# Performance work log

Measured on AMD Instinct MI355X. Metric: run time of the kernel, lower is better.

Reference implementation:

```python
import jax, jax.numpy as jnp
import numpy as np

EPS = 1e-5

def _bn(h):
    # BatchNorm1d, affine=False, track_running_stats=False -> batch stats, biased var
    m = h.mean(axis=0)
    v = h.var(axis=0)
    return (h - m) * jax.lax.rsqrt(v + EPS)

def _aggregate(x, edge_index):
    # out[i] = sum over edges (i <- j) of x[j]  + x[i] (self loop)
    dst, src = edge_index[0], edge_index[1]
    n = x.shape[0]
    return jax.ops.segment_sum(x[src], dst, num_segments=n) + x

def setup_inputs() -> dict:
    key = jax.random.key(0)
    ks = jax.random.split(key, 12)
    N, F, H, C, E = 100000, 128, 128, 40, 800000
    x = jax.random.normal(ks[0], (N, F), dtype=jnp.float32)
    edge_index = jax.random.randint(ks[1], (2, E), 0, N, dtype=jnp.int64)
    def lin(kw, kb, fan_in, fan_out):
        bound = 1.0 / np.sqrt(fan_in)
        W = jax.random.uniform(kw, (fan_in, fan_out), minval=-bound, maxval=bound, dtype=jnp.float32)
        b = jax.random.uniform(kb, (fan_out,), minval=-bound, maxval=bound, dtype=jnp.float32)
        return W, b
    W0, b0 = lin(ks[2], ks[3], F, H)
    W1, b1 = lin(ks[4], ks[5], H, H)
    W2, b2 = lin(ks[6], ks[7], H, H)
    Wl, bl = lin(ks[8], ks[9], H, C)
    return {"x": x, "edge_index": edge_index, "W0": W0, "b0": b0,
            "W1": W1, "b1": b1, "W2": W2, "b2": b2, "Wl": Wl, "bl": bl}

def reference(x, edge_index, W0, b0, W1, b1, W2, b2, Wl, bl):
    h = x
    for W, b in ((W0, b0), (W1, b1), (W2, b2)):
        h = _aggregate(h, edge_index)          # spmm(A + I, h)
        h = h @ W + b                          # Linear
        h = _bn(h)                             # BatchNorm1d (no affine)
        h = jax.nn.relu(h)
    return h @ Wl + bl
```

## Files before the change

kernel.cpp:

```cpp
#include <hip/hip_runtime.h>
#include <stdint.h>

typedef __attribute__((ext_vector_type(8))) short short8;
typedef __attribute__((ext_vector_type(4))) float floatx4;

static __device__ __forceinline__ float b2f(uint16_t b){
    return __uint_as_float(((uint32_t)b) << 16);
}
static __device__ __forceinline__ uint16_t f2b(float f){
    uint32_t u = __float_as_uint(f);
    return (uint16_t)((u + 0x7fffu + ((u >> 16) & 1u)) >> 16);
}
static __device__ __forceinline__ float blo(uint32_t v){ return __uint_as_float(v << 16); }
static __device__ __forceinline__ float bhi(uint32_t v){ return __uint_as_float(v & 0xffff0000u); }
static __device__ __forceinline__ uint32_t pack2(float a, float b){
    return ((uint32_t)f2b(b) << 16) | (uint32_t)f2b(a);
}

__global__ void k_sentinel(uint32_t* out, int nwords, uint32_t pat){
    int i = blockIdx.x * blockDim.x + threadIdx.x;
    if (i < nwords) out[i] = pat;
}

__global__ void k_zf(int* deg, int N, const uint32_t* xw, const int* ei, int* flags,
                     float* stats, int ZB){
    if ((int)blockIdx.x == ZB){
        if (threadIdx.x != 0) return;
        int odd_nz = 0;
        for (int k = 0; k < 128; k++){
            if (ei[2 * k + 1] != 0) odd_nz = 1;
        }
        flags[0] = odd_nz ? 0 : 1;
        int big = 0;
        for (int k = 0; k < 128; k++){
            float lo = __uint_as_float(xw[k] << 16);
            if (!(fabsf(lo) <= 1024.0f)) big = 1;
        }
        flags[1] = big ? 0 : 1;
        return;
    }
    if ((int)blockIdx.x == ZB + 1){
        int t = threadIdx.x;
        #pragma unroll
        for (int j = 0; j < 3; j++) stats[j * 256 + t] = 0.f;
        return;
    }
    int i = blockIdx.x * blockDim.x + threadIdx.x;
    if (i < N) deg[i] = 0;
}

__global__ void k_deg(const int* ei, int E, int* deg, uint16_t* rank, const int* flags){
    int e = blockIdx.x * blockDim.x + threadIdx.x;
    if (e < E){
        int d = flags[0] ? ei[2 * e] : ei[e];
        int r = atomicAdd(&deg[d], 1);
        rank[e] = (uint16_t)r;
    }
}

__global__ void k_scan1(const int* deg, int N, int* bsum){
    __shared__ int s[256];
    int t = threadIdx.x;
    int i = blockIdx.x * 256 + t;
    s[t] = (i < N) ? deg[i] : 0;
    __syncthreads();
    for (int off = 128; off > 0; off >>= 1){
        if (t < off) s[t] += s[t + off];
        __syncthreads();
    }
    if (t == 0) bsum[blockIdx.x] = s[0];
}

__global__ void k_scan2(int* bsum, int nb, int* rp, int N){
    __shared__ int s[512];
    int t = threadIdx.x;
    int v = (t < nb) ? bsum[t] : 0;
    s[t] = v;
    __syncthreads();
    for (int off = 1; off < 512; off <<= 1){
        int u = (t >= off) ? s[t - off] : 0;
        __syncthreads();
        s[t] += u;
        __syncthreads();
    }
    if (t < nb) bsum[t] = s[t] - v;
    if (t == 511) rp[N] = s[511];
}

__global__ void k_scan3(const int* deg, int N, const int* bpre, int* rp){
    __shared__ int s[256];
    int t = threadIdx.x;
    int i = blockIdx.x * 256 + t;
    int v = (i < N) ? deg[i] : 0;
    s[t] = v;
    __syncthreads();
    for (int off = 1; off < 256; off <<= 1){
        int u = (t >= off) ? s[t - off] : 0;
        __syncthreads();
        s[t] += u;
        __syncthreads();
    }
    if (i < N) rp[i] = bpre[blockIdx.x] + s[t] - v;
}

__global__ __launch_bounds__(256) void k_fill(const int* __restrict__ ei, int E,
                                              const int* __restrict__ rp,
                                              const uint16_t* __restrict__ rank,
                                              int* __restrict__ col,
                                              const int* __restrict__ flags, int N){
    int xcd = blockIdx.x & 7;
    int sub = blockIdx.x >> 3;
    int nsub = gridDim.x >> 3;
    int r0 = (int)(((long long)N * xcd) >> 3);
    int r1 = (int)(((long long)N * (xcd + 1)) >> 3);
    int e0 = (int)(((long long)E * sub) / nsub);
    int e1 = (int)(((long long)E * (sub + 1)) / nsub);
    int is64 = flags[0];
    for (int e = e0 + threadIdx.x; e < e1; e += 256){
        int d = is64 ? ei[2 * e] : ei[e];
        if (d >= r0 && d < r1){
            int sv = is64 ? ei[2 * (E + e)] : ei[E + e];
            int p = rp[d] + (int)rank[e];
            col[p] = sv;
        }
    }
}

__global__ void k_prep(const void* W0, const void* W1, const void* W2, const void* Wl,
                       uint16_t* Wf0, uint16_t* Wf1, uint16_t* Wf2, uint16_t* Wfl,
                       const void* b0, const void* b1, const void* b2, const void* bl,
                       float* bc, const void* x, uint16_t* hx, int N,
                       const int* flags){
    int blk = blockIdx.x;
    int t = threadIdx.x;
    if (blk >= 218){
        int nb = gridDim.x - 218;
        int bi = blk - 218;
        int half2 = N * 2;
        int isbf = flags[1];
        for (int c = 0; c < 8; c++){
            uint4* dst = (uint4*)(hx + (size_t)c * N * 16);
            if (isbf){
                const uint16_t* xb = (const uint16_t*)x;
                for (int idx = bi * 256 + t; idx < half2; idx += nb * 256){
                    int row = idx >> 1, h = idx & 1;
                    dst[idx] = *(const uint4*)(xb + (size_t)row * 128 + c * 16 + h * 8);
                }
            } else {
                const float* xf = (const float*)x;
                for (int idx = bi * 256 + t; idx < half2; idx += nb * 256){
                    int row = idx >> 1, h = idx & 1;
                    const float4* s = (const float4*)(xf + (size_t)row * 128 + c * 16 + h * 8);
                    float4 u0 = s[0];
                    float4 u1 = s[1];
                    uint4 o;
                    o.x = pack2(u0.x, u0.y); o.y = pack2(u0.z, u0.w);
                    o.z = pack2(u1.x, u1.y); o.w = pack2(u1.z, u1.w);
                    dst[idx] = o;
                }
            }
        }
        return;
    }
    if (blk >= 216){
        int i = (blk - 216) * 256 + t;
        if (i >= 424) return;
        const void* src; int li;
        if (i < 128)      { src = b0; li = i; }
        else if (i < 256) { src = b1; li = i - 128; }
        else if (i < 384) { src = b2; li = i - 256; }
        else              { src = bl; li = i - 384; }
        bc[i] = flags[1] ? b2f(((const uint16_t*)src)[li]) : ((const float*)src)[li];
        return;
    }
    const void* W; uint16_t* Wf; int C, ntiles, lb;
    if (blk < 64)        { W = W0; Wf = Wf0; C = 128; ntiles = 8; lb = blk; }
    else if (blk < 128)  { W = W1; Wf = Wf1; C = 128; ntiles = 8; lb = blk - 64; }
    else if (blk < 192)  { W = W2; Wf = Wf2; C = 128; ntiles = 8; lb = blk - 128; }
    else                 { W = Wl; Wf = Wfl; C = 40;  ntiles = 3; lb = blk - 192; }
    int idx = lb * 256 + t;
    int total = 4 * ntiles * 512;
    if (idx >= total) return;
    int j = idx & 7;
    int lane = (idx >> 3) & 63;
    int nt = (idx >> 9) % ntiles;
    int kt = idx / (512 * ntiles);
    int k = kt * 32 + (lane >> 4) * 8 + j;
    int n = nt * 16 + (lane & 15);
    uint16_t v = 0;
    if (n < C){
        v = flags[1] ? ((const uint16_t*)W)[k * C + n]
                     : f2b(((const float*)W)[k * C + n]);
    }
    Wf[idx] = v;
}

__global__ __launch_bounds__(256) void k_aggc(const uint16_t* __restrict__ Yin,
                                              const int* __restrict__ rp,
                                              const int* __restrict__ col,
                                              uint16_t* __restrict__ out,
                                              int N, int RT,
                                              const float* __restrict__ st,
                                              int apply_bn, float ninv){
    int t = threadIdx.x;
    int c = blockIdx.x & 7;
    int tile = blockIdx.x >> 3;
    int r = t >> 1, h = t & 1;
    int i = tile * 128 + r;
    if (i >= N) return;
    float tt[8], iv[8];
    if (apply_bn){
        int f0 = c * 16 + h * 8;
        #pragma unroll
        for (int j = 0; j < 8; j++){
            float sv = st[f0 + j];
            float qv = st[128 + f0 + j];
            float m = sv * ninv;
            float var = qv * ninv - m * m;
            float ivj = rsqrtf(var + 1e-5f);
            iv[j] = ivj;
            tt[j] = -m * ivj;
        }
    }
    const uint4* base = (const uint4*)(Yin + (size_t)c * N * 16);
    int s0 = rp[i], e0 = rp[i + 1];
    float a[8];
    {
        uint4 w = base[(size_t)i * 2 + h];
        a[0] = blo(w.x); a[1] = bhi(w.x); a[2] = blo(w.y); a[3] = bhi(w.y);
        a[4] = blo(w.z); a[5] = bhi(w.z); a[6] = blo(w.w); a[7] = bhi(w.w);
        if (apply_bn){
            #pragma unroll
            for (int jj = 0; jj < 8; jj++) a[jj] = fmaxf(fmaf(a[jj], iv[jj], tt[jj]), 0.f);
        }
    }
    int k = s0;
    for (; k + 3 < e0; k += 4){
        int j0 = col[k], j1 = col[k + 1], j2 = col[k + 2], j3 = col[k + 3];
        uint4 ww[4];
        ww[0] = base[(size_t)j0 * 2 + h];
        ww[1] = base[(size_t)j1 * 2 + h];
        ww[2] = base[(size_t)j2 * 2 + h];
        ww[3] = base[(size_t)j3 * 2 + h];
        #pragma unroll
        for (int u = 0; u < 4; u++){
            float v[8] = {blo(ww[u].x), bhi(ww[u].x), blo(ww[u].y), bhi(ww[u].y),
                          blo(ww[u].z), bhi(ww[u].z), blo(ww[u].w), bhi(ww[u].w)};
            if (apply_bn){
                #pragma unroll
                for (int jj = 0; jj < 8; jj++) v[jj] = fmaxf(fmaf(v[jj], iv[jj], tt[jj]), 0.f);
            }
            #pragma unroll
            for (int jj = 0; jj < 8; jj++) a[jj] += v[jj];
        }
    }
    for (; k < e0; k++){
        int j = col[k];
        uint4 w = base[(size_t)j * 2 + h];
        float v[8] = {blo(w.x), bhi(w.x), blo(w.y), bhi(w.y),
                      blo(w.z), bhi(w.z), blo(w.w), bhi(w.w)};
        if (apply_bn){
            #pragma unroll
            for (int jj = 0; jj < 8; jj++) v[jj] = fmaxf(fmaf(v[jj], iv[jj], tt[jj]), 0.f);
        }
        #pragma unroll
        for (int jj = 0; jj < 8; jj++) a[jj] += v[jj];
    }
    uint4 o;
    o.x = pack2(a[0], a[1]); o.y = pack2(a[2], a[3]);
    o.z = pack2(a[4], a[5]); o.w = pack2(a[6], a[7]);
    ((uint4*)(out + (size_t)c * N * 16))[(size_t)i * 2 + h] = o;
}

__global__ __launch_bounds__(256) void k_gemm(uint16_t* __restrict__ A,
                                              const uint16_t* __restrict__ Wf,
                                              const float* __restrict__ bias,
                                              float* __restrict__ part, int N){
    __shared__ __align__(16) uint16_t wlds[16384];
    __shared__ float sh_sum[128], sh_ssq[128];
    int t = threadIdx.x;
    if (t < 128){ sh_sum[t] = 0.f; sh_ssq[t] = 0.f; }
    {
        const uint4* s = (const uint4*)Wf;
        uint4* d = (uint4*)wlds;
        for (int i = t; i < 2048; i += 256) d[i] = s[i];
    }
    __syncthreads();
    int lane = t & 63, wave = t >> 6;
    int m = lane & 15, q = lane >> 4;
    int rb[2];
    rb[0] = blockIdx.x * 128 + wave * 16;
    rb[1] = rb[0] + 64;
    short8 afrag[2][4];
    #pragma unroll
    for (int mt = 0; mt < 2; mt++){
        int arow = rb[mt] + m;
        if (arow >= N) arow = N - 1;
        #pragma unroll
        for (int kt = 0; kt < 4; kt++){
            int cc = 2 * kt + (q >> 1);
            afrag[mt][kt] = *(const short8*)(A + (size_t)cc * N * 16
                                               + (size_t)arow * 16 + (q & 1) * 8);
        }
    }
    floatx4 acc[2][8];
    #pragma unroll
    for (int mt = 0; mt < 2; mt++)
        #pragma unroll
        for (int nt = 0; nt < 8; nt++) acc[mt][nt] = (floatx4){0.f, 0.f, 0.f, 0.f};
    const short8* wl = (const short8*)wlds;
    #pragma unroll
    for (int kt = 0; kt < 4; kt++){
        #pragma unroll
        for (int nt = 0; nt < 8; nt++){
            short8 bfrag = wl[(kt * 8 + nt) * 64 + lane];
            #pragma unroll
            for (int mt = 0; mt < 2; mt++){
                acc[mt][nt] = __builtin_amdgcn_mfma_f32_16x16x32_bf16(afrag[mt][kt], bfrag, acc[mt][nt], 0, 0, 0);
            }
        }
    }
    #pragma unroll
    for (int mt = 0; mt < 2; mt++){
        #pragma unroll
        for (int nt = 0; nt < 8; nt++){
            int ccol = nt * 16 + m;
            float bv = bias[ccol];
            float s = 0.f, ss = 0.f;
            #pragma unroll
            for (int r = 0; r < 4; r++){
                int grow = rb[mt] + q * 4 + r;
                if (grow < N){
                    float y = acc[mt][nt][r] + bv;
                    A[(size_t)nt * N * 16 + (size_t)grow * 16 + m] = f2b(y);
                    s += y;
                    ss += y * y;
                }
            }
            s += __shfl_xor(s, 16); s += __shfl_xor(s, 32);
            ss += __shfl_xor(ss, 16); ss += __shfl_xor(ss, 32);
            if (q == 0){
                atomicAdd(&sh_sum[ccol], s);
                atomicAdd(&sh_ssq[ccol], ss);
            }
        }
    }
    __syncthreads();
    if (t < 128){
        part[(size_t)blockIdx.x * 256 + t] = sh_sum[t];
        part[(size_t)blockIdx.x * 256 + 128 + t] = sh_ssq[t];
    }
}

__global__ __launch_bounds__(256) void k_red(const float* __restrict__ part, int nb,
                                             float* __restrict__ st){
    int t = threadIdx.x;
    int r0 = blockIdx.x * 32;
    int r1 = r0 + 32; if (r1 > nb) r1 = nb;
    float s0 = 0.f, s1 = 0.f, s2 = 0.f, s3 = 0.f;
    int b = r0;
    for (; b + 3 < r1; b += 4){
        s0 += part[(size_t)b * 256 + t];
        s1 += part[(size_t)(b + 1) * 256 + t];
        s2 += part[(size_t)(b + 2) * 256 + t];
        s3 += part[(size_t)(b + 3) * 256 + t];
    }
    for (; b < r1; b++) s0 += part[(size_t)b * 256 + t];
    atomicAdd(&st[t], (s0 + s1) + (s2 + s3));
}

__global__ __launch_bounds__(256) void k_out(const uint16_t* __restrict__ A,
                                             const uint16_t* __restrict__ Wf,
                                             const float* __restrict__ bias,
                                             const float* __restrict__ st, float ninv,
                                             void* __restrict__ out, int N,
                                             const int* __restrict__ flags){
    __shared__ __align__(16) uint16_t wlds[6144];
    __shared__ float s_m[128], s_iv[128];
    int t = threadIdx.x;
    {
        const uint4* s = (const uint4*)Wf;
        uint4* d = (uint4*)wlds;
        for (int i = t; i < 768; i += 256) d[i] = s[i];
    }
    if (t < 128){
        float m = st[t] * ninv;
        float var = st[128 + t] * ninv - m * m;
        s_m[t] = m;
        s_iv[t] = rsqrtf(var + 1e-5f);
    }
    __syncthreads();
    int lane = t & 63, wave = t >> 6;
    int m = lane & 15, q = lane >> 4;
    int row_base = blockIdx.x * 64 + wave * 16;
    int arow = row_base + m;
    if (arow >= N) arow = N - 1;
    short8 afrag[4];
    #pragma unroll
    for (int kt = 0; kt < 4; kt++){
        uint4 u = *(const uint4*)(A + (size_t)(2 * kt + (q >> 1)) * N * 16
                                    + (size_t)arow * 16 + (q & 1) * 8);
        float v[8] = {blo(u.x), bhi(u.x), blo(u.y), bhi(u.y),
                      blo(u.z), bhi(u.z), blo(u.w), bhi(u.w)};
        int c0 = kt * 32 + q * 8;
        #pragma unroll
        for (int j = 0; j < 8; j++) v[j] = fmaxf((v[j] - s_m[c0 + j]) * s_iv[c0 + j], 0.f);
        uint4 o;
        o.x = pack2(v[0], v[1]); o.y = pack2(v[2], v[3]);
        o.z = pack2(v[4], v[5]); o.w = pack2(v[6], v[7]);
        afrag[kt] = *(short8*)&o;
    }
    floatx4 acc[3];
    #pragma unroll
    for (int nt = 0; nt < 3; nt++) acc[nt] = (floatx4){0.f, 0.f, 0.f, 0.f};
    const short8* wl = (const short8*)wlds;
    #pragma unroll
    for (int kt = 0; kt < 4; kt++){
        #pragma unroll
        for (int nt = 0; nt < 3; nt++){
            acc[nt] = __builtin_amdgcn_mfma_f32_16x16x32_bf16(afrag[kt], wl[(kt * 3 + nt) * 64 + lane], acc[nt], 0, 0, 0);
        }
    }
    int isbf = flags[1];
    #pragma unroll
    for (int nt = 0; nt < 3; nt++){
        int ccol = nt * 16 + m;
        if (ccol < 40){
            float bv = bias[ccol];
            #pragma unroll
            for (int r = 0; r < 4; r++){
                int grow = row_base + q * 4 + r;
                if (grow < N){
                    float y = acc[nt][r] + bv;
                    if (isbf) ((uint16_t*)out)[(size_t)grow * 40 + ccol] = f2b(y);
                    else      ((float*)out)[(size_t)grow * 40 + ccol] = y;
                }
            }
        }
    }
}

extern "C" void kernel_launch(void* const* d_in, const int* in_sizes, int n_in,
                              void* d_out, int out_size, void* d_ws, size_t ws_size,
                              hipStream_t stream){
    (void)n_in;
    const void* x  = d_in[0];
    const int* ei  = (const int*)d_in[1];
    const void* W0 = d_in[2];
    const void* b0 = d_in[3];
    const void* W1 = d_in[4];
    const void* b1 = d_in[5];
    const void* W2 = d_in[6];
    const void* b2 = d_in[7];
    const void* Wl = d_in[8];
    const void* bl = d_in[9];

    const int N = in_sizes[0] / 128;
    const int E = in_sizes[1] / 2;
    const int NF = N * 128;
    const int NB = (N + 255) / 256;
    const int RT = (N + 127) / 128;
    const int aggc_grid    = 8 * RT;
    const int gemm_blocks2 = RT;
    const int gemm_blocks  = (N + 63) / 64;
    const int red_blocks   = (gemm_blocks2 + 31) / 32;

    char* ws = (char*)d_ws;
    size_t off = 0;
    uint16_t* hx = (uint16_t*)(ws + off); off += ((size_t)NF * 2 + 255) & ~(size_t)255;
    uint16_t* ag = (uint16_t*)(ws + off); off += ((size_t)NF * 2 + 255) & ~(size_t)255;
    int* col     = (int*)(ws + off);      off += ((size_t)E * 4 + 255) & ~(size_t)255;
    int* rp      = (int*)(ws + off);      off += ((size_t)(N + 1) * 4 + 255) & ~(size_t)255;
    uint16_t* rank = (uint16_t*)(ws + off); off += ((size_t)E * 2 + 255) & ~(size_t)255;
    int* deg     = (int*)(ws + off);      off += ((size_t)N * 4 + 255) & ~(size_t)255;
    int* bsum    = (int*)(ws + off);      off += 512 * 4;
    int* flags   = (int*)(ws + off);      off += 256;
    uint16_t* Wf0 = (uint16_t*)(ws + off); off += 16384 * 2;
    uint16_t* Wf1 = (uint16_t*)(ws + off); off += 16384 * 2;
    uint16_t* Wf2 = (uint16_t*)(ws + off); off += 16384 * 2;
    uint16_t* Wfl = (uint16_t*)(ws + off); off += 6144 * 2;
    float* bc    = (float*)(ws + off);    off += 424 * 4 + 160;
    float* stats = (float*)(ws + off);    off += 768 * 4;
    float* part  = (float*)(ws + off);    off += (size_t)gemm_blocks2 * 256 * 4;
    const size_t required = off;

    if (ws_size < required){
        int nwords = out_size / 2;
        k_sentinel<<<(nwords + 255) / 256, 256, 0, stream>>>((uint32_t*)d_out, nwords, 0x40004000u);
        return;
    }

    k_zf<<<NB + 2, 256, 0, stream>>>(deg, N, (const uint32_t*)x, ei, flags, stats, NB);
    k_deg<<<(E + 255) / 256, 256, 0, stream>>>(ei, E, deg, rank, flags);
    k_scan1<<<NB, 256, 0, stream>>>(deg, N, bsum);
    k_scan2<<<1, 512, 0, stream>>>(bsum, NB, rp, N);
    k_scan3<<<NB, 256, 0, stream>>>(deg, N, bsum, rp);
    k_fill<<<1024, 256, 0, stream>>>(ei, E, rp, rank, col, flags, N);

    k_prep<<<2266, 256, 0, stream>>>(W0, W1, W2, Wl, Wf0, Wf1, Wf2, Wfl,
                                     b0, b1, b2, bl, bc, x, hx, N, flags);

    const float ninv = 1.0f / (float)N;

    k_aggc<<<aggc_grid, 256, 0, stream>>>(hx, rp, col, ag, N, RT, stats, 0, ninv);
    k_gemm<<<gemm_blocks2, 256, 0, stream>>>(ag, Wf0, bc, part, N);
    k_red<<<red_blocks, 256, 0, stream>>>(part, gemm_blocks2, stats);
    k_aggc<<<aggc_grid, 256, 0, stream>>>(ag, rp, col, hx, N, RT, stats, 1, ninv);
    k_gemm<<<gemm_blocks2, 256, 0, stream>>>(hx, Wf1, bc + 128, part, N);
    k_red<<<red_blocks, 256, 0, stream>>>(part, gemm_blocks2, stats + 256);
    k_aggc<<<aggc_grid, 256, 0, stream>>>(hx, rp, col, ag, N, RT, stats + 256, 1, ninv);
    k_gemm<<<gemm_blocks2, 256, 0, stream>>>(ag, Wf2, bc + 256, part, N);
    k_red<<<red_blocks, 256, 0, stream>>>(part, gemm_blocks2, stats + 512);
    k_out<<<gemm_blocks, 256, 0, stream>>>(ag, Wfl, bc + 384, stats + 512, ninv, d_out, N, flags);
}
```

Before: 408.1 us.

## Sort rows by in-degree bucket to balance aggregation warp workloads

Adds a degree histogram, built during the first scan pass, and a counting-sort kernel that produces a permutation of nodes grouped by in-degree. The aggregation kernel now processes rows in this permuted order, so threads in a wavefront have similar edge counts and suffer less divergence. The cost is an extra kernel, extra atomics and an indirection load per row. Neighbouring threads now handle non-contiguous rows, so output writes become scattered.

```diff
diff --git a/kernel.cpp b/kernel.cpp
--- a/kernel.cpp
+++ b/kernel.cpp
@@ -23,7 +23,7 @@
 }
 
 __global__ void k_zf(int* deg, int N, const uint32_t* xw, const int* ei, int* flags,
-                     float* stats, int ZB){
+                     float* stats, int* hist, int ZB){
     if ((int)blockIdx.x == ZB){
         if (threadIdx.x != 0) return;
         int odd_nz = 0;
@@ -43,6 +43,7 @@
         int t = threadIdx.x;
         #pragma unroll
         for (int j = 0; j < 3; j++) stats[j * 256 + t] = 0.f;
+        if (t < 64) hist[t] = 0;
         return;
     }
     int i = blockIdx.x * blockDim.x + threadIdx.x;
@@ -58,20 +59,29 @@
     }
 }
 
-__global__ void k_scan1(const int* deg, int N, int* bsum){
+__global__ void k_scan1(const int* deg, int N, int* bsum, int* hist){
     __shared__ int s[256];
-    int t = threadIdx.x;
+    __shared__ int lh[64];
+    int t = threadIdx.x;
+    if (t < 64) lh[t] = 0;
     int i = blockIdx.x * 256 + t;
-    s[t] = (i < N) ? deg[i] : 0;
-    __syncthreads();
+    int dv = (i < N) ? deg[i] : 0;
+    s[t] = dv;
+    __syncthreads();
+    if (i < N){
+        int b = dv < 63 ? dv : 63;
+        atomicAdd(&lh[b], 1);
+    }
     for (int off = 128; off > 0; off >>= 1){
         if (t < off) s[t] += s[t + off];
         __syncthreads();
     }
     if (t == 0) bsum[blockIdx.x] = s[0];
-}
-
-__global__ void k_scan2(int* bsum, int nb, int* rp, int N){
+    if (t < 64 && lh[t]) atomicAdd(&hist[t], lh[t]);
+}
+
+__global__ void k_scan2(int* bsum, int nb, int* rp, int N,
+                        const int* hist, int* hcur){
     __shared__ int s[512];
     int t = threadIdx.x;
     int v = (t < nb) ? bsum[t] : 0;
@@ -85,6 +95,14 @@
     }
     if (t < nb) bsum[t] = s[t] - v;
     if (t == 511) rp[N] = s[511];
+    if (t == 0){
+        int acc = 0;
+        for (int b = 0; b < 64; b++){
+            int c = hist[b];
+            hcur[b] = acc;
+            acc += c;
+        }
+    }
 }
 
 __global__ void k_scan3(const int* deg, int N, const int* bpre, int* rp){
@@ -101,6 +119,28 @@
         __syncthreads();
     }
     if (i < N) rp[i] = bpre[blockIdx.x] + s[t] - v;
+}
+
+__global__ void k_perm(const int* __restrict__ deg, int N, int* __restrict__ hcur,
+                       int* __restrict__ perm){
+    __shared__ int lcnt[64], lbase[64], lcur[64];
+    int t = threadIdx.x;
+    if (t < 64){ lcnt[t] = 0; lcur[t] = 0; }
+    __syncthreads();
+    int i = blockIdx.x * 256 + t;
+    int b = -1;
+    if (i < N){
+        int dv = deg[i];
+        b = dv < 63 ? dv : 63;
+        atomicAdd(&lcnt[b], 1);
+    }
+    __syncthreads();
+    if (t < 64 && lcnt[t] > 0) lbase[t] = atomicAdd(&hcur[t], lcnt[t]);
+    __syncthreads();
+    if (i < N){
+        int r = atomicAdd(&lcur[b], 1);
+        perm[lbase[b] + r] = i;
+    }
 }
 
 __global__ __launch_bounds__(256) void k_fill(const int* __restrict__ ei, int E,
@@ -198,6 +238,7 @@
 __global__ __launch_bounds__(256) void k_aggc(const uint16_t* __restrict__ Yin,
                                               const int* __restrict__ rp,
                                               const int* __restrict__ col,
+                                              const int* __restrict__ perm,
                                               uint16_t* __restrict__ out,
                                               int N, int RT,
                                               const float* __restrict__ st,
@@ -206,8 +247,9 @@
     int c = blockIdx.x & 7;
     int tile = blockIdx.x >> 3;
     int r = t >> 1, h = t & 1;
-    int i = tile * 128 + r;
-    if (i >= N) return;
+    int idx = tile * 128 + r;
+    if (idx >= N) return;
+    int i = perm[idx];
     float tt[8], iv[8];
     if (apply_bn){
         int f0 = c * 16 + h * 8;
@@ -473,8 +515,11 @@
     int* rp      = (int*)(ws + off);      off += ((size_t)(N + 1) * 4 + 255) & ~(size_t)255;
     uint16_t* rank = (uint16_t*)(ws + off); off += ((size_t)E * 2 + 255) & ~(size_t)255;
     int* deg     = (int*)(ws + off);      off += ((size_t)N * 4 + 255) & ~(size_t)255;
+    int* perm    = (int*)(ws + off);      off += ((size_t)N * 4 + 255) & ~(size_t)255;
     int* bsum    = (int*)(ws + off);      off += 512 * 4;
     int* flags   = (int*)(ws + off);      off += 256;
+    int* hist    = (int*)(ws + off);      off += 64 * 4;
+    int* hcur    = (int*)(ws + off);      off += 64 * 4 + 128;
     uint16_t* Wf0 = (uint16_t*)(ws + off); off += 16384 * 2;
     uint16_t* Wf1 = (uint16_t*)(ws + off); off += 16384 * 2;
     uint16_t* Wf2 = (uint16_t*)(ws + off); off += 16384 * 2;
@@ -490,11 +535,12 @@
         return;
     }
 
-    k_zf<<<NB + 2, 256, 0, stream>>>(deg, N, (const uint32_t*)x, ei, flags, stats, NB);
+    k_zf<<<NB + 2, 256, 0, stream>>>(deg, N, (const uint32_t*)x, ei, flags, stats, hist, NB);
     k_deg<<<(E + 255) / 256, 256, 0, stream>>>(ei, E, deg, rank, flags);
-    k_scan1<<<NB, 256, 0, stream>>>(deg, N, bsum);
-    k_scan2<<<1, 512, 0, stream>>>(bsum, NB, rp, N);
+    k_scan1<<<NB, 256, 0, stream>>>(deg, N, bsum, hist);
+    k_scan2<<<1, 512, 0, stream>>>(bsum, NB, rp, N, hist, hcur);
     k_scan3<<<NB, 256, 0, stream>>>(deg, N, bsum, rp);
+    k_perm<<<NB, 256, 0, stream>>>(deg, N, hcur, perm);
     k_fill<<<1024, 256, 0, stream>>>(ei, E, rp, rank, col, flags, N);
 
     k_prep<<<2266, 256, 0, stream>>>(W0, W1, W2, Wl, Wf0, Wf1, Wf2, Wfl,
@@ -502,13 +548,13 @@
 
     const float ninv = 1.0f / (float)N;
 
-    k_aggc<<<aggc_grid, 256, 0, stream>>>(hx, rp, col, ag, N, RT, stats, 0, ninv);
+    k_aggc<<<aggc_grid, 256, 0, stream>>>(hx, rp, col, perm, ag, N, RT, stats, 0, ninv);
     k_gemm<<<gemm_blocks2, 256, 0, stream>>>(ag, Wf0, bc, part, N);
     k_red<<<red_blocks, 256, 0, stream>>>(part, gemm_blocks2, stats);
-    k_aggc<<<aggc_grid, 256, 0, stream>>>(ag, rp, col, hx, N, RT, stats, 1, ninv);
+    k_aggc<<<aggc_grid, 256, 0, stream>>>(ag, rp, col, perm, hx, N, RT, stats, 1, ninv);
     k_gemm<<<gemm_blocks2, 256, 0, stream>>>(hx, Wf1, bc + 128, part, N);
     k_red<<<red_blocks, 256, 0, stream>>>(part, gemm_blocks2, stats + 256);
-    k_aggc<<<aggc_grid, 256, 0, stream>>>(hx, rp, col, ag, N, RT, stats + 256, 1, ninv);
+    k_aggc<<<aggc_grid, 256, 0, stream>>>(hx, rp, col, perm, ag, N, RT, stats + 256, 1, ninv);
     k_gemm<<<gemm_blocks2, 256, 0, stream>>>(ag, Wf2, bc + 256, part, N);
     k_red<<<red_blocks, 256, 0, stream>>>(part, gemm_blocks2, stats + 512);
     k_out<<<gemm_blocks, 256, 0, stream>>>(ag, Wfl, bc + 384, stats + 512, ninv, d_out, N, flags);
```

Measured after the change: 509.4 us. 24.8% more time.
